# Optimization experiments

Measured on AMD Instinct MI355X. Metric: run time of the kernel, lower is better.

Reference implementation:

```python
import jax, jax.numpy as jnp
import numpy as np

DIM, FFN, GC, NSET, K = 48, 2, 2, 32, 3
HID = DIM * FFN          # 96 hidden features
G = HID // GC            # 48 groups in KBA
CG = HID // G            # 2 channels per group
INTERC = 24              # min(dim, 24)
B, H, W = 4, 128, 128


def _conv(x, w, b=None, groups=1, pad=0):
    out = jax.lax.conv_general_dilated(
        x, w, (1, 1), [(pad, pad), (pad, pad)],
        dimension_numbers=('NCHW', 'OIHW', 'NCHW'),
        feature_group_count=groups)
    if b is not None:
        out = out + b[None, :, None, None]
    return out


def _kba(x, att, k, g, bb, ww):
    # x: [B,c,H,W], att: [B,nset,H,W], bb: [1,nset,c], ww: [1,nset,c*c//g*k*k]
    Bz, c, Hh, Ww = x.shape
    KK = k * k
    cg = c // g
    P = Hh * Ww
    a = att.reshape(Bz, -1, P).transpose(0, 2, 1)                     # [B,P,nset]
    bias = jnp.einsum('bpn,nc->bpc', a, bb[0])                        # [B,P,c]
    attk = jnp.einsum('bpn,nm->bpm', a, ww[0]).reshape(Bz, P, g, cg, cg * KK)
    pd = k // 2
    xp = jnp.pad(x, ((0, 0), (0, 0), (pd, pd), (pd, pd)))
    # im2col patches, torch.unfold layout: channel-major, kernel row-major
    patches = jnp.stack([xp[:, :, i:i + Hh, j:j + Ww]
                         for i in range(k) for j in range(k)], axis=2)  # [B,c,KK,H,W]
    uf = patches.reshape(Bz, g, cg * KK, P).transpose(0, 3, 1, 2)       # [B,P,g,cg*KK]
    out = jnp.einsum('bpgom,bpgm->bpgo', attk, uf).reshape(Bz, P, c) + bias
    return out.transpose(0, 2, 1).reshape(Bz, c, Hh, Ww)


def setup_inputs() -> dict:
    key = jax.random.key(0)
    ks = jax.random.split(key, 20)
    s = 0.05
    inp = {
        'x': jax.random.normal(ks[0], (B, DIM, H, W), jnp.float32),
        'dw1_w': jax.random.normal(ks[1], (HID, DIM, 1, 1), jnp.float32) * s,
        'dw2_w': jax.random.normal(ks[2], (HID, 1, 3, 3), jnp.float32) * s,
        'proj_w': jax.random.normal(ks[3], (DIM, HID, 1, 1), jnp.float32) * s,
        'sca_w': jax.random.normal(ks[4], (HID, HID, 1, 1), jnp.float32) * s,
        'sca_b': jax.random.normal(ks[5], (HID,), jnp.float32) * s,
        'c1_w1': jax.random.normal(ks[6], (HID, DIM, 1, 1), jnp.float32) * s,
        'c1_w2': jax.random.normal(ks[7], (HID, 1, 3, 3), jnp.float32) * s,
        'kba_w': jax.random.normal(ks[8], (1, NSET, HID * CG * K * K), jnp.float32) * s,
        'kba_b': jax.random.normal(ks[9], (1, NSET, HID), jnp.float32) * s,
        'c2_w1': jax.random.normal(ks[10], (INTERC, DIM // INTERC, 3, 3), jnp.float32) * s,
        'c2_b1': jax.random.normal(ks[11], (INTERC,), jnp.float32) * s,
        'c2_w2': jax.random.normal(ks[12], (NSET, INTERC // 2, 1, 1), jnp.float32) * s,
        'c2_b2': jax.random.normal(ks[13], (NSET,), jnp.float32) * s,
        'c211_w': jax.random.normal(ks[14], (NSET, DIM, 1, 1), jnp.float32) * s,
        'c211_b': jax.random.normal(ks[15], (NSET,), jnp.float32) * s,
        'attgamma': jnp.full((1, NSET, 1, 1), 0.01, jnp.float32),
        'ga1': jnp.full((1, HID, 1, 1), 0.01, jnp.float32),
    }
    return inp


def reference(x, dw1_w, dw2_w, proj_w, sca_w, sca_b, c1_w1, c1_w2,
              kba_w, kba_b, c2_w1, c2_b1, c2_w2, c2_b2,
              c211_w, c211_b, attgamma, ga1):
    # dwconv branch: 1x1 -> depthwise 3x3
    x1 = _conv(_conv(x, dw1_w), dw2_w, groups=HID, pad=1)
    # attention map branch: grouped 3x3 -> SimpleGate -> 1x1, scaled + skip 1x1
    t = _conv(x, c2_w1, c2_b1, groups=INTERC, pad=1)
    t1, t2 = jnp.split(t, 2, axis=1)
    t = _conv(t1 * t2, c2_w2, c2_b2)
    att = t * attgamma + _conv(x, c211_w, c211_b)
    # conv1 branch feeding KBA
    uf = _conv(_conv(x, c1_w1), c1_w2, groups=HID, pad=1)
    x2 = _kba(uf, att, K, G, kba_b, kba_w) * ga1 + uf
    comb = jax.nn.gelu(x1, approximate=False) * x2
    pooled = jnp.mean(comb, axis=(2, 3), keepdims=True)
    comb = comb * _conv(pooled, sca_w, sca_b)
    return _conv(comb, proj_w)
```

## Files before the change

kernel.cpp:

```cpp
#include <hip/hip_runtime.h>
#include <math.h>

#define BB 4
#define HH 128
#define WW 128
#define HWP (HH*WW)
#define DIMC 48
#define HIDC 96
#define NSETC 32

#define XS_W 27
#define HS_W 102
#define US_W 102

typedef __attribute__((ext_vector_type(8))) short bf16x8;
typedef __attribute__((ext_vector_type(4))) float f32x4;
typedef __attribute__((ext_vector_type(2))) float f32x2;

static __device__ __forceinline__ unsigned short f2bf(float f) {
    union { float f; unsigned u; } v; v.f = f;
    unsigned r = (v.u + 0x7FFFu + ((v.u >> 16) & 1u)) >> 16;
    return (unsigned short)r;
}
static __device__ __forceinline__ unsigned rnd_bf(float f) {
    union { float f; unsigned u; } v; v.f = f;
    return v.u + 0x8000u;
}
static __device__ __forceinline__ unsigned pack2bf(float lo, float hi) {
    return __builtin_amdgcn_perm(rnd_bf(hi), rnd_bf(lo), 0x07060302u);
}
static __device__ __forceinline__ void st_bf_hi(unsigned short* p, float f) {
    *p = (unsigned short)(rnd_bf(f) >> 16);
}
static __device__ __forceinline__ float bf2f(unsigned short u) {
    union { unsigned u; float f; } v; v.u = ((unsigned)u) << 16;
    return v.f;
}
static __device__ __forceinline__ float bfpair_lo(unsigned pr) {
    union { unsigned u; float f; } v; v.u = pr << 16; return v.f;
}
static __device__ __forceinline__ float bfpair_hi(unsigned pr) {
    union { unsigned u; float f; } v; v.u = pr & 0xffff0000u; return v.f;
}
static __device__ __forceinline__ float gelu(float x) {
    return 0.5f * x * (1.0f + erff(x * 0.70710678118654752f));
}

__global__ __launch_bounds__(256) void k_prep(
    const float* __restrict__ x,
    const float* __restrict__ kbaw, const float* __restrict__ kbab,
    const float* __restrict__ dw1w, const float* __restrict__ c1w1,
    const float* __restrict__ ga1,  const float* __restrict__ c211w,
    const float* __restrict__ c2w2, const float* __restrict__ c2b2,
    const float* __restrict__ c211b, const float* __restrict__ attg,
    unsigned short* __restrict__ Bpk, unsigned short* __restrict__ Bpw,
    unsigned short* __restrict__ Aps, unsigned short* __restrict__ Ag,
    unsigned* __restrict__ x_p, float* __restrict__ pooled)
{
    __shared__ unsigned ts[256 * 26];
    int blk = blockIdx.x, tid = threadIdx.x;
    if (blk < 300) {
        int t = blk * 256 + tid;
        if (t < 61440) {
            int j = t & 7, lane = (t >> 3) & 63, tile = t >> 9;
            int chunk = tile / 10, nt = tile - chunk * 10;
            int m = lane & 15, qn = lane >> 4;
            int lc = 4 * nt + (m & 3);
            int o = lc / 20, tt = lc % 20;
            int c = (m >> 2) * 24 + 2 * chunk + o;
            int n = qn * 8 + j;
            float v = 0.f;
            if (tt < 18)       v = kbaw[n * 1728 + (c >> 1) * 36 + (c & 1) * 18 + tt] * ga1[c];
            else if (tt == 18) v = kbab[n * 96 + c] * ga1[c];
            Bpk[t] = f2bf(v);
        } else if (t < 73728) {
            int u = t - 61440;
            int s = u / 6144;
            int rem = u % 6144;
            int nt = rem >> 9;
            int lane = (rem >> 3) & 63, j = rem & 7;
            int k = s * 32 + ((lane >> 4) << 3) + j;
            int col = (nt << 4) + (lane & 15);
            float v = 0.f;
            if (k < 48) v = (col < 96) ? dw1w[col * 48 + k] : c1w1[(col - 96) * 48 + k];
            Bpw[u] = f2bf(v);
        } else if (t < 75776) {
            int u = t - 73728;
            int j = u & 7, lane = (u >> 3) & 63, tile = u >> 9;
            int kt = tile >> 1, nt2 = tile & 1;
            int m = lane & 15, qn = lane >> 4;
            int n = 8 * (m >> 2) + 4 * nt2 + (m & 3);
            int k = kt * 32 + qn * 8 + j;
            Aps[u] = f2bf(k < 48 ? c211w[n * 48 + k] : 0.f);
        } else if (t < 76800) {
            int u = t - 75776;
            int j = u & 7, lane = (u >> 3) & 63, nt2 = u >> 9;
            int m = lane & 15, qn = lane >> 4;
            int n = 8 * (m >> 2) + 4 * nt2 + (m & 3);
            int k = qn * 8 + j;
            float v = 0.f;
            if (k < 12)       v = c2w2[n * 12 + k] * attg[n];
            else if (k == 12) v = c2b2[n] * attg[n] + c211b[n];
            Ag[u] = f2bf(v);
        }
    } else {
        int xblk = blk - 300;
        if (xblk == 0) {
            for (int i = tid; i < BB * HIDC; i += 256) pooled[i] = 0.f;
        }
        int b = xblk >> 6;
        int p0 = (xblk & 63) << 8;
        const float* xb = x + (size_t)b * DIMC * HWP + p0;
        #pragma unroll
        for (int c2 = 0; c2 < 24; ++c2) {
            float lo = xb[(2 * c2) * HWP + tid];
            float hi = xb[(2 * c2 + 1) * HWP + tid];
            ts[tid * 26 + c2] = pack2bf(lo, hi);
        }
        __syncthreads();
        unsigned* dst = x_p + ((size_t)b * HWP + p0) * 24;
        for (int idx = tid; idx < 256 * 24; idx += 256) {
            int px = idx / 24, j2 = idx - px * 24;
            dst[px * 24 + j2] = ts[px * 26 + j2];
        }
    }
}

__global__ __launch_bounds__(512, 4) void k_mff(
    const unsigned* __restrict__ x_p,
    const uint4* __restrict__ BpkA, const uint4* __restrict__ Bpw,
    const uint4* __restrict__ Aps,  const uint4* __restrict__ Ag,
    const float* __restrict__ c1w2, const float* __restrict__ dw2w,
    const float* __restrict__ c2w1, const float* __restrict__ c2b1,
    unsigned* __restrict__ comb_bf, float* __restrict__ pooled)
{
    __shared__ __attribute__((aligned(16))) unsigned xs[144 * XS_W];
    __shared__ __attribute__((aligned(16))) unsigned short hsw[144 * HS_W];
    __shared__ unsigned short us2p[100 * US_W];
    __shared__ float wls[864 + 432 + 24];
    __shared__ float pooled_s[96];

    int lane = threadIdx.x, wy = threadIdx.y;
    int tid = wy * 64 + lane;
    int blk = blockIdx.x;
    int b = blk >> 8, ty = (blk >> 4) & 15, tx = blk & 15;
    int q = lane >> 4, i16 = lane & 15;
    int wh = wy >> 2;
    int wp = wy & 3;

    float* wats  = wls + 864;
    float* c2b1s = wls + 864 + 432;
    float* att_tf = (float*)hsw;

    if (tid < 96) pooled_s[tid] = 0.f;
    for (int idx = tid; idx < 864; idx += 512) {
        int t5 = idx / 96, c = idx - t5 * 96;
        wls[idx] = dw2w[c * 9 + t5];
    }
    for (int idx = tid; idx < 216; idx += 512) {
        int g = idx / 9, tap = idx - g * 9;
        wats[idx * 2]     = c2w1[g * 18 + tap];
        wats[idx * 2 + 1] = c2w1[g * 18 + 9 + tap];
    }
    if (tid < 24) c2b1s[tid] = c2b1[tid];
    for (int idx = tid; idx < 144 * 12; idx += 512) {
        int pos = idx / 12, jp = idx - pos * 12;
        int gy = ty * 8 - 2 + pos / 12, gx = tx * 8 - 2 + pos % 12;
        uint2 v = {0u, 0u};
        if (((unsigned)gy < (unsigned)HH) & ((unsigned)gx < (unsigned)WW))
            v = *(const uint2*)&x_p[((size_t)b * HWP + gy * WW + gx) * 24 + jp * 2];
        xs[pos * XS_W + jp * 2]     = v.x;
        xs[pos * XS_W + jp * 2 + 1] = v.y;
    }
    __syncthreads();

    int p_t = wp * 16 + i16;
    int pyT = p_t >> 3, pxT = p_t & 7;
    int gp = (ty * 8 + pyT) * WW + tx * 8 + pxT;
    uint4 z4 = {0u, 0u, 0u, 0u};

    #pragma unroll
    for (int ci = 0; ci < 3; ++ci) {
        int g = q * 6 + wh * 3 + ci;
        float acc = c2b1s[g];
        #pragma unroll
        for (int di = 0; di < 3; ++di)
          #pragma unroll
          for (int dj = 0; dj < 3; ++dj) {
              unsigned pr = xs[((pyT + 1 + di) * 12 + pxT + 1 + dj) * XS_W + g];
              f32x2 w2 = *(const f32x2*)&wats[(g * 9 + di * 3 + dj) * 2];
              acc += w2.x * bfpair_lo(pr) + w2.y * bfpair_hi(pr);
          }
        att_tf[p_t * XS_W + g] = acc;
    }
    __syncthreads();

    bf16x8 afrag;
    {
        int p26 = p_t * XS_W;
        unsigned tgd[4];
        #pragma unroll
        for (int i2 = 0; i2 < 4; ++i2) {
            int k0 = q * 8 + 2 * i2;
            int k1 = k0 + 1;
            float v0 = (k0 < 12) ? att_tf[p26 + k0] * att_tf[p26 + 12 + k0] : (k0 == 12 ? 1.f : 0.f);
            float v1 = (k1 < 12) ? att_tf[p26 + k1] * att_tf[p26 + 12 + k1] : (k1 == 12 ? 1.f : 0.f);
            tgd[i2] = pack2bf(v0, v1);
        }
        uint4 tgr = {tgd[0], tgd[1], tgd[2], tgd[3]};
        bf16x8 btg = __builtin_bit_cast(bf16x8, tgr);

        int cen = (pyT + 2) * 12 + (pxT + 2);
        int cb = cen * XS_W + q * 4;
        uint4 bx0r = {xs[cb], xs[cb + 1], xs[cb + 2], xs[cb + 3]};
        uint4 bx1r = z4;
        if (q < 2) {
            int cb2 = cen * XS_W + 16 + q * 4;
            bx1r.x = xs[cb2]; bx1r.y = xs[cb2 + 1]; bx1r.z = xs[cb2 + 2]; bx1r.w = xs[cb2 + 3];
        }
        bf16x8 bx0 = __builtin_bit_cast(bf16x8, bx0r);
        bf16x8 bx1 = __builtin_bit_cast(bf16x8, bx1r);

        float attv[8];
        #pragma unroll
        for (int nt2 = 0; nt2 < 2; ++nt2) {
            bf16x8 ag  = __builtin_bit_cast(bf16x8, Ag[nt2 * 64 + lane]);
            bf16x8 as0 = __builtin_bit_cast(bf16x8, Aps[nt2 * 64 + lane]);
            bf16x8 as1 = __builtin_bit_cast(bf16x8, Aps[(2 + nt2) * 64 + lane]);
            f32x4 z = {0.f, 0.f, 0.f, 0.f};
            f32x4 c = __builtin_amdgcn_mfma_f32_16x16x32_bf16(ag, btg, z, 0, 0, 0);
            c = __builtin_amdgcn_mfma_f32_16x16x32_bf16(as1, bx1, c, 0, 0, 0);
            c = __builtin_amdgcn_mfma_f32_16x16x32_bf16(as0, bx0, c, 0, 0, 0);
            #pragma unroll
            for (int r = 0; r < 4; ++r) attv[nt2 * 4 + r] = c[r];
        }
        uint4 au = {pack2bf(attv[0], attv[1]), pack2bf(attv[2], attv[3]),
                    pack2bf(attv[4], attv[5]), pack2bf(attv[6], attv[7])};
        afrag = __builtin_bit_cast(bf16x8, au);
    }
    __syncthreads();

    {
        {
            int rg = wy;
            int hp = rg * 16 + i16;
            int ab = hp * XS_W + q * 4;
            uint4 a0r = {xs[ab], xs[ab + 1], xs[ab + 2], xs[ab + 3]};
            uint4 a1r = z4;
            if (q < 2) {
                int ab2 = hp * XS_W + 16 + q * 4;
                a1r.x = xs[ab2]; a1r.y = xs[ab2 + 1]; a1r.z = xs[ab2 + 2]; a1r.w = xs[ab2 + 3];
            }
            bf16x8 a0 = __builtin_bit_cast(bf16x8, a0r);
            bf16x8 a1 = __builtin_bit_cast(bf16x8, a1r);
            int rowb = rg * 16 + 4 * q;
            #pragma unroll
            for (int nt = 0; nt < 6; ++nt) {
                bf16x8 b0 = __builtin_bit_cast(bf16x8, Bpw[(size_t)((6 + nt) << 6) + lane]);
                bf16x8 b1 = __builtin_bit_cast(bf16x8, Bpw[(size_t)((18 + nt) << 6) + lane]);
                f32x4 z = {0.f, 0.f, 0.f, 0.f};
                f32x4 c = __builtin_amdgcn_mfma_f32_16x16x32_bf16(a1, b1, z, 0, 0, 0);
                c = __builtin_amdgcn_mfma_f32_16x16x32_bf16(a0, b0, c, 0, 0, 0);
                #pragma unroll
                for (int r = 0; r < 4; ++r)
                    st_bf_hi(&hsw[(rowb + r) * HS_W + nt * 16 + i16], c[r]);
            }
        }
        if (wy >= 1 && wy <= 6) {
            int hp = 128 + i16;
            int ab = hp * XS_W + q * 4;
            uint4 a0r = {xs[ab], xs[ab + 1], xs[ab + 2], xs[ab + 3]};
            uint4 a1r = z4;
            if (q < 2) {
                int ab2 = hp * XS_W + 16 + q * 4;
                a1r.x = xs[ab2]; a1r.y = xs[ab2 + 1]; a1r.z = xs[ab2 + 2]; a1r.w = xs[ab2 + 3];
            }
            bf16x8 a0 = __builtin_bit_cast(bf16x8, a0r);
            bf16x8 a1 = __builtin_bit_cast(bf16x8, a1r);
            int rowb = 128 + 4 * q;
            int nt = wy - 1;
            bf16x8 b0 = __builtin_bit_cast(bf16x8, Bpw[(size_t)((6 + nt) << 6) + lane]);
            bf16x8 b1 = __builtin_bit_cast(bf16x8, Bpw[(size_t)((18 + nt) << 6) + lane]);
            f32x4 z = {0.f, 0.f, 0.f, 0.f};
            f32x4 c = __builtin_amdgcn_mfma_f32_16x16x32_bf16(a1, b1, z, 0, 0, 0);
            c = __builtin_amdgcn_mfma_f32_16x16x32_bf16(a0, b0, c, 0, 0, 0);
            #pragma unroll
            for (int r = 0; r < 4; ++r)
                st_bf_hi(&hsw[(rowb + r) * HS_W + nt * 16 + i16], c[r]);
        }
    }
    __syncthreads();

    #pragma unroll 1
    for (int it = 0; it < 3; ++it) {
        int su = wy * 3 + it;
        int cq = su >> 1;
        const float* w9 = c1w2 + cq * 8 * 9;
        int hp2 = (su & 1) * 50 + lane;
        if (lane < 50) {
            int py2 = hp2 / 10, px2 = hp2 - py2 * 10;
            float acc[8];
            #pragma unroll
            for (int c = 0; c < 8; ++c) acc[c] = 0.f;
            #pragma unroll
            for (int di = 0; di < 3; ++di)
              #pragma unroll
              for (int dj = 0; dj < 3; ++dj) {
                  int rb = ((py2 + di) * 12 + px2 + dj) * HS_W + cq * 8;
                  unsigned pp[4];
                  pp[0] = *(const unsigned*)&hsw[rb];
                  pp[1] = *(const unsigned*)&hsw[rb + 2];
                  pp[2] = *(const unsigned*)&hsw[rb + 4];
                  pp[3] = *(const unsigned*)&hsw[rb + 6];
                  #pragma unroll
                  for (int c2 = 0; c2 < 4; ++c2) {
                      acc[2*c2]   += w9[(2*c2) * 9 + di * 3 + dj]   * bfpair_lo(pp[c2]);
                      acc[2*c2+1] += w9[(2*c2+1) * 9 + di * 3 + dj] * bfpair_hi(pp[c2]);
                  }
              }
            int wb = hp2 * US_W + cq * 8;
            *(unsigned*)&us2p[wb]     = pack2bf(acc[0], acc[1]);
            *(unsigned*)&us2p[wb + 2] = pack2bf(acc[2], acc[3]);
            *(unsigned*)&us2p[wb + 4] = pack2bf(acc[4], acc[5]);
            *(unsigned*)&us2p[wb + 6] = pack2bf(acc[6], acc[7]);
        }
    }
    __syncthreads();

    if (wy < 7) {
        int rg = wy;
        int hp = rg * 16 + i16;
        bool okp = hp < 100;
        int hy = hp / 10, hx = hp - hy * 10;
        int pos = okp ? ((hy + 1) * 12 + hx + 1) : 0;
        int ab = pos * XS_W + q * 4;
        uint4 a0r = {xs[ab], xs[ab + 1], xs[ab + 2], xs[ab + 3]};
        uint4 a1r = z4;
        if (q < 2) {
            int ab2 = pos * XS_W + 16 + q * 4;
            a1r.x = xs[ab2]; a1r.y = xs[ab2 + 1]; a1r.z = xs[ab2 + 2]; a1r.w = xs[ab2 + 3];
        }
        bf16x8 a0 = __builtin_bit_cast(bf16x8, a0r);
        bf16x8 a1 = __builtin_bit_cast(bf16x8, a1r);
        int rowb = rg * 16 + 4 * q;
        #pragma unroll
        for (int nt = 0; nt < 6; ++nt) {
            bf16x8 b0 = __builtin_bit_cast(bf16x8, Bpw[(size_t)(nt << 6) + lane]);
            bf16x8 b1 = __builtin_bit_cast(bf16x8, Bpw[(size_t)((12 + nt) << 6) + lane]);
            f32x4 z = {0.f, 0.f, 0.f, 0.f};
            f32x4 c = __builtin_amdgcn_mfma_f32_16x16x32_bf16(a1, b1, z, 0, 0, 0);
            c = __builtin_amdgcn_mfma_f32_16x16x32_bf16(a0, b0, c, 0, 0, 0);
            #pragma unroll
            for (int r = 0; r < 4; ++r)
                st_bf_hi(&hsw[(rowb + r) * HS_W + nt * 16 + i16], c[r]);
        }
    }
    __syncthreads();

    f32x2 greg[6];
    {
        int base = q * 24 + wh * 12;
        #pragma unroll
        for (int cc = 0; cc < 6; ++cc) {
            int c0 = base + 2 * cc;
            f32x2 acc = {0.f, 0.f};
            #pragma unroll
            for (int di = 0; di < 3; ++di)
              #pragma unroll
              for (int dj = 0; dj < 3; ++dj) {
                  unsigned pr = *(const unsigned*)&hsw[((pyT + di) * 10 + pxT + dj) * HS_W + c0];
                  f32x2 hv = {bfpair_lo(pr), bfpair_hi(pr)};
                  f32x2 wv = *(const f32x2*)&wls[(di * 3 + dj) * 96 + c0];
                  acc += wv * hv;
              }
            greg[cc].x = gelu(acc.x);
            greg[cc].y = gelu(acc.y);
        }
    }

    unsigned* cmb = comb_bf + ((size_t)b * HWP + gp) * 48 + q * 12;
    int hpC = (pyT + 1) * 10 + pxT + 1;
    const uint4* bpk_base = BpkA + (size_t)(wh * 60) * 64 + lane;

    uint4 buf[2][10];
    #pragma unroll
    for (int nt = 0; nt < 10; ++nt) buf[0][nt] = bpk_base[(size_t)nt << 6];

    #pragma unroll
    for (int cl = 0; cl < 6; ++cl) {
        int chunk = wh * 6 + cl;
        if (cl < 5) {
            #pragma unroll
            for (int nt = 0; nt < 10; ++nt)
                buf[(cl + 1) & 1][nt] = bpk_base[(size_t)(((cl + 1) * 10 + nt)) << 6];
        }
        int c0 = q * 24 + 2 * chunk;
        float u[18];
        #pragma unroll
        for (int i = 0; i < 3; ++i)
          #pragma unroll
          for (int j = 0; j < 3; ++j) {
              unsigned pr = *(const unsigned*)&us2p[((pyT + i) * 10 + pxT + j) * US_W + c0];
              u[i * 3 + j]     = bfpair_lo(pr);
              u[9 + i * 3 + j] = bfpair_hi(pr);
          }
        unsigned sp = *(const unsigned*)&us2p[hpC * US_W + c0];
        f32x4 cf[10];
        #pragma unroll
        for (int nt = 0; nt < 10; ++nt) {
            bf16x8 aW = __builtin_bit_cast(bf16x8, buf[cl & 1][nt]);
            f32x4 z = {0.f, 0.f, 0.f, 0.f};
            cf[nt] = __builtin_amdgcn_mfma_f32_16x16x32_bf16(aW, afrag, z, 0, 0, 0);
        }
        float acc0 = cf[4][2];
        float acc1 = cf[9][2];
        #pragma unroll
        for (int m = 0; m < 16; ++m) {
            acc0 += cf[m >> 2][m & 3]       * u[m];
            acc1 += cf[5 + (m >> 2)][m & 3] * u[m];
        }
        acc0 += cf[4][0] * u[16] + cf[4][1] * u[17];
        acc1 += cf[9][0] * u[16] + cf[9][1] * u[17];

        float x20 = acc0 + bfpair_lo(sp);
        float x21 = acc1 + bfpair_hi(sp);
        float cv0 = greg[cl].x * x20;
        float cv1 = greg[cl].y * x21;
        cmb[chunk] = pack2bf(cv0, cv1);
        float r0 = cv0, r1 = cv1;
        #pragma unroll
        for (int s = 1; s < 16; s <<= 1) {
            r0 += __shfl_xor(r0, s, 64);
            r1 += __shfl_xor(r1, s, 64);
        }
        if (i16 == 0) {
            atomicAdd(&pooled_s[c0], r0);
            atomicAdd(&pooled_s[c0 + 1], r1);
        }
    }
    __syncthreads();
    if (tid < 96) atomicAdd(&pooled[b * HIDC + tid], pooled_s[tid]);
}

__global__ __launch_bounds__(256) void k_final(
    const unsigned* __restrict__ comb_bf, const float* __restrict__ pooled,
    const float* __restrict__ scaw, const float* __restrict__ scab,
    const float* __restrict__ projw, float* __restrict__ out)
{
    __shared__ float svs[96];
    __shared__ float cs[96][66];
    int tid = threadIdx.x;
    int blk = blockIdx.x;
    int p0 = blk * 64;
    int b = p0 >> 14;
    if (tid < 96) {
        float dot = 0.f;
        const float* pr = pooled + b * 96;
        const float* wr = scaw + tid * 96;
        #pragma unroll 4
        for (int k = 0; k < 96; ++k) dot += wr[k] * pr[k];
        svs[tid] = scab[tid] + dot * (1.0f / (float)HWP);
    }
    __syncthreads();
    for (int idx = tid; idx < 64 * 12; idx += 256) {
        int px = idx / 12, cq = idx - px * 12;
        uint4 v = *(const uint4*)&comb_bf[(size_t)(p0 + px) * 48 + cq * 4];
        int k0 = cq * 8;
        unsigned pp[4] = {v.x, v.y, v.z, v.w};
        #pragma unroll
        for (int j = 0; j < 4; ++j) {
            cs[k0 + 2*j][px]     = bfpair_lo(pp[j]) * svs[k0 + 2*j];
            cs[k0 + 2*j + 1][px] = bfpair_hi(pp[j]) * svs[k0 + 2*j + 1];
        }
    }
    __syncthreads();
    int l = tid & 63, w = tid >> 6;
    int o0 = w * 12;
    float acc[12];
    #pragma unroll
    for (int o = 0; o < 12; ++o) acc[o] = 0.f;
    #pragma unroll 4
    for (int k = 0; k < 96; ++k) {
        float v = cs[k][l];
        #pragma unroll
        for (int o = 0; o < 12; ++o)
            acc[o] += projw[(o0 + o) * 96 + k] * v;
    }
    float* ob = out + (size_t)b * DIMC * HWP + (p0 & 16383) + l;
    #pragma unroll
    for (int o = 0; o < 12; ++o)
        ob[(o0 + o) * HWP] = acc[o];
}

extern "C" void kernel_launch(void* const* d_in, const int* in_sizes, int n_in,
                              void* d_out, int out_size, void* d_ws, size_t ws_size,
                              hipStream_t stream)
{
    const float* x     = (const float*)d_in[0];
    const float* dw1w  = (const float*)d_in[1];
    const float* dw2w  = (const float*)d_in[2];
    const float* projw = (const float*)d_in[3];
    const float* scaw  = (const float*)d_in[4];
    const float* scab  = (const float*)d_in[5];
    const float* c1w1  = (const float*)d_in[6];
    const float* c1w2  = (const float*)d_in[7];
    const float* kbaw  = (const float*)d_in[8];
    const float* kbab  = (const float*)d_in[9];
    const float* c2w1  = (const float*)d_in[10];
    const float* c2b1  = (const float*)d_in[11];
    const float* c2w2  = (const float*)d_in[12];
    const float* c2b2  = (const float*)d_in[13];
    const float* c211w = (const float*)d_in[14];
    const float* c211b = (const float*)d_in[15];
    const float* attg  = (const float*)d_in[16];
    const float* ga1   = (const float*)d_in[17];

    unsigned* x_p     = (unsigned*)d_ws;
    unsigned* comb_bf = x_p + (size_t)BB * HWP * 24;
    float* pooled     = (float*)(comb_bf + (size_t)BB * HWP * 48);
    unsigned short* BpkA = (unsigned short*)(pooled + BB * HIDC);
    unsigned short* Bpw  = BpkA + 61440;
    unsigned short* Aps  = Bpw + 12288;
    unsigned short* Ag   = Aps + 2048;

    k_prep <<<556,  256, 0, stream>>>(x, kbaw, kbab, dw1w, c1w1, ga1, c211w, c2w2, c2b2,
                                      c211b, attg, BpkA, Bpw, Aps, Ag, x_p, pooled);
    k_mff  <<<1024, dim3(64,8,1), 0, stream>>>(x_p, (const uint4*)BpkA, (const uint4*)Bpw,
                                               (const uint4*)Aps, (const uint4*)Ag,
                                               c1w2, dw2w, c2w1, c2b1, comb_bf, pooled);
    k_final<<<1024, 256, 0, stream>>>(comb_bf, pooled, scaw, scab, projw, (float*)d_out);
}
```

Baseline: 212.9 us.

## Stage KBA weight fragments into LDS via async global-to-LDS loads

Replaces the per-wave double-buffered register prefetch of the KBA weight tiles with global_load_lds DMA into a double-buffered LDS region that reuses the xs/hsw shared pool. Each block loads the tiles once, shared by all waves, instead of every wave fetching its own copy into registers. The goal is to cut redundant global traffic and free many VGPRs. It adds a __syncthreads per chunk iteration and relaxes launch bounds from 4 to 2 blocks per CU, which may lower occupancy. Correctness also depends on the DMA writes finishing before the barrier.

```diff
diff --git a/kernel.cpp b/kernel.cpp
--- a/kernel.cpp
+++ b/kernel.cpp
@@ -32,10 +32,6 @@
 static __device__ __forceinline__ void st_bf_hi(unsigned short* p, float f) {
     *p = (unsigned short)(rnd_bf(f) >> 16);
 }
-static __device__ __forceinline__ float bf2f(unsigned short u) {
-    union { unsigned u; float f; } v; v.u = ((unsigned)u) << 16;
-    return v.f;
-}
 static __device__ __forceinline__ float bfpair_lo(unsigned pr) {
     union { unsigned u; float f; } v; v.u = pr << 16; return v.f;
 }
@@ -44,6 +40,11 @@
 }
 static __device__ __forceinline__ float gelu(float x) {
     return 0.5f * x * (1.0f + erff(x * 0.70710678118654752f));
+}
+static __device__ __forceinline__ void gll16(const void* g, void* l) {
+    __builtin_amdgcn_global_load_lds(
+        (const __attribute__((address_space(1))) void*)g,
+        (__attribute__((address_space(3))) void*)l, 16, 0, 0);
 }
 
 __global__ __launch_bounds__(256) void k_prep(
@@ -126,7 +127,7 @@
     }
 }
 
-__global__ __launch_bounds__(512, 4) void k_mff(
+__global__ __launch_bounds__(512, 2) void k_mff(
     const unsigned* __restrict__ x_p,
     const uint4* __restrict__ BpkA, const uint4* __restrict__ Bpw,
     const uint4* __restrict__ Aps,  const uint4* __restrict__ Ag,
@@ -134,11 +135,13 @@
     const float* __restrict__ c2w1, const float* __restrict__ c2b1,
     unsigned* __restrict__ comb_bf, float* __restrict__ pooled)
 {
-    __shared__ __attribute__((aligned(16))) unsigned xs[144 * XS_W];
-    __shared__ __attribute__((aligned(16))) unsigned short hsw[144 * HS_W];
+    __shared__ __attribute__((aligned(16))) unsigned smem_pool[144 * XS_W + (144 * HS_W) / 2];
     __shared__ unsigned short us2p[100 * US_W];
     __shared__ float wls[864 + 432 + 24];
     __shared__ float pooled_s[96];
+
+    unsigned* xs = smem_pool;
+    unsigned short* hsw = (unsigned short*)(smem_pool + 144 * XS_W);
 
     int lane = threadIdx.x, wy = threadIdx.y;
     int tid = wy * 64 + lane;
@@ -378,23 +381,38 @@
         }
     }
 
+    __syncthreads();
+
+    char* kst = (char*)smem_pool;
+    const char* bsrc = (const char*)BpkA;
+    {
+        #pragma unroll
+        for (int s = wy; s < 20; s += 8) {
+            int half = (s >= 10) ? 1 : 0;
+            int tile = s - half * 10;
+            gll16(bsrc + ((half * 6) * 10 + tile) * 1024 + lane * 16, kst + s * 1024);
+        }
+    }
+
     unsigned* cmb = comb_bf + ((size_t)b * HWP + gp) * 48 + q * 12;
     int hpC = (pyT + 1) * 10 + pxT + 1;
-    const uint4* bpk_base = BpkA + (size_t)(wh * 60) * 64 + lane;
-
-    uint4 buf[2][10];
-    #pragma unroll
-    for (int nt = 0; nt < 10; ++nt) buf[0][nt] = bpk_base[(size_t)nt << 6];
 
     #pragma unroll
     for (int cl = 0; cl < 6; ++cl) {
+        __syncthreads();
+        if (cl < 5) {
+            #pragma unroll
+            for (int s = wy; s < 20; s += 8) {
+                int half = (s >= 10) ? 1 : 0;
+                int tile = s - half * 10;
+                gll16(bsrc + ((half * 6 + cl + 1) * 10 + tile) * 1024 + lane * 16,
+                      kst + ((cl + 1) & 1) * 20480 + s * 1024);
+            }
+        }
         int chunk = wh * 6 + cl;
-        if (cl < 5) {
-            #pragma unroll
-            for (int nt = 0; nt < 10; ++nt)
-                buf[(cl + 1) & 1][nt] = bpk_base[(size_t)(((cl + 1) * 10 + nt)) << 6];
-        }
         int c0 = q * 24 + 2 * chunk;
+        const uint4* bl = (const uint4*)(kst + (cl & 1) * 20480 + wh * 10240);
+
         float u[18];
         #pragma unroll
         for (int i = 0; i < 3; ++i)
@@ -408,7 +426,7 @@
         f32x4 cf[10];
         #pragma unroll
         for (int nt = 0; nt < 10; ++nt) {
-            bf16x8 aW = __builtin_bit_cast(bf16x8, buf[cl & 1][nt]);
+            bf16x8 aW = __builtin_bit_cast(bf16x8, bl[nt * 64 + lane]);
             f32x4 z = {0.f, 0.f, 0.f, 0.f};
             cf[nt] = __builtin_amdgcn_mfma_f32_16x16x32_bf16(aW, afrag, z, 0, 0, 0);
         }
```

Measured after the change: 204.0 us. 4.2% less time.
